# Kernel tuning notes

Hardware: AMD Instinct MI355X
Metric: run time of the kernel (lower is better)

## Reference

```python
import jax, jax.numpy as jnp
import numpy as np

N = 50000          # nodes
E = 800000         # edges (COO)
IN_CH = 128
H1, H2, OUT = 200, 100, 2   # 100*out, 50*out, out with out_channels=2
EPS = 1e-12
DROP_P = 0.1


def setup_inputs() -> dict:
    key = jax.random.key(0)
    ks = jax.random.split(key, 6)
    x = jax.random.normal(ks[0], (N, IN_CH), dtype=jnp.float32)
    edge_index = jax.random.randint(ks[1], (2, E), 0, N)
    W1 = jax.random.normal(ks[2], (IN_CH, H1), dtype=jnp.float32) / np.sqrt(IN_CH)
    W2 = jax.random.normal(ks[3], (H1, H2), dtype=jnp.float32) / np.sqrt(H1)
    W3 = jax.random.normal(ks[4], (H2, OUT), dtype=jnp.float32) / np.sqrt(H2)
    beta1 = jnp.float32(1.0)
    beta2 = jnp.float32(1.0)
    beta3 = jnp.float32(1.0)
    return dict(x=x, edge_index=edge_index, W1=W1, W2=W2, W3=W3,
                beta1=beta1, beta2=beta2, beta3=beta3)


def _agnn_layer(x, W, beta, src, dst):
    # project in -> out channels, then AGNN cosine-attention propagation
    h = x @ W                                               # [N, D]
    hn = h / jnp.maximum(jnp.linalg.norm(h, axis=-1, keepdims=True), EPS)
    a = beta * jnp.sum(hn[src] * hn[dst], axis=-1)          # [E'] edge logits
    amax = jax.ops.segment_max(a, dst, num_segments=N)      # stable segment softmax
    amax = jnp.where(jnp.isfinite(amax), amax, 0.0)
    e = jnp.exp(a - amax[dst])
    denom = jax.ops.segment_sum(e, dst, num_segments=N)
    alpha = e / jnp.maximum(denom[dst], EPS)
    return jax.ops.segment_sum(h[src] * alpha[:, None], dst, num_segments=N)


def _dropout(k, x, p=DROP_P):
    keep = jax.random.bernoulli(k, 1.0 - p, x.shape)
    return jnp.where(keep, x / (1.0 - p), 0.0)


def reference(x, edge_index, W1, W2, W3, beta1, beta2, beta3):
    src, dst = edge_index[0], edge_index[1]
    loop = jnp.arange(N)                                    # self-loops (AGNNConv default)
    src = jnp.concatenate([src, loop])
    dst = jnp.concatenate([dst, loop])
    k1, k2 = jax.random.split(jax.random.key(42))
    h = jax.nn.relu(_agnn_layer(x, W1, beta1, src, dst))
    h = _dropout(k1, h)
    h = jax.nn.relu(_agnn_layer(h, W2, beta2, src, dst))
    h = _dropout(k2, h)
    h = jax.nn.relu(_agnn_layer(h, W3, beta3, src, dst))
    return h
```

## Files before the change

### kernel.cpp

```cpp
#include <hip/hip_runtime.h>
#include <hip/hip_bf16.h>

#define NN 50000
#define NE 800000
#define EPSN 1e-12f


#define H_OFF    0ull
#define A_OFF    40000000ull
#define H3_OFF   80000000ull
#define RINV_OFF 80400000ull
#define OFFS_OFF 80600000ull
#define DEG_OFF  80800016ull
#define CURS_OFF 81000016ull
#define ESRC_OFF 81200016ull
#define CHNK_OFF 84600016ull

__host__ __device__ inline void tf20(unsigned k0, unsigned k1, unsigned& x0, unsigned& x1) {
  unsigned ks2 = k0 ^ k1 ^ 0x1BD11BDAu;
  x0 += k0; x1 += k1;
#define TFR(r) { x0 += x1; x1 = ((x1 << (r)) | (x1 >> (32 - (r)))) ^ x0; }
  TFR(13) TFR(15) TFR(26) TFR(6)
  x0 += k1;  x1 += ks2 + 1u;
  TFR(17) TFR(29) TFR(16) TFR(24)
  x0 += ks2; x1 += k0 + 2u;
  TFR(13) TFR(15) TFR(26) TFR(6)
  x0 += k0;  x1 += k1 + 3u;
  TFR(17) TFR(29) TFR(16) TFR(24)
  x0 += k1;  x1 += ks2 + 4u;
  TFR(13) TFR(15) TFR(26) TFR(6)
  x0 += ks2; x1 += k0 + 5u;
#undef TFR
}

__device__ __forceinline__ float dropf(float val, unsigned k0, unsigned k1, unsigned i) {
  unsigned x0 = 0u, x1 = i;
  tf20(k0, k1, x0, x1);
  unsigned bits = x0 ^ x1;
  float u = __uint_as_float((bits >> 9) | 0x3F800000u) - 1.0f;
  return (u < 0.9f) ? val * (1.0f / 0.9f) : 0.0f;
}

__device__ __forceinline__ float wave_sum(float x) {
  x += __shfl_xor(x, 32); x += __shfl_xor(x, 16); x += __shfl_xor(x, 8);
  x += __shfl_xor(x, 4);  x += __shfl_xor(x, 2);  x += __shfl_xor(x, 1);
  return x;
}

__global__ __launch_bounds__(256) void csr_hist_kernel(const int* __restrict__ ei, int* __restrict__ deg) {
  int e = blockIdx.x * 256 + threadIdx.x;
  if (e >= NE) return;
  atomicAdd(&deg[ei[NE + e]], 1);
}

__global__ __launch_bounds__(256) void csr_scan1_kernel(const int* __restrict__ deg,
                                                        int* __restrict__ offs,
                                                        int* __restrict__ chunk) {
  __shared__ int lds[8];
  int t = threadIdx.x;
  int base = blockIdx.x * 1024 + t * 4;
  int d[4];
#pragma unroll
  for (int j = 0; j < 4; j++) d[j] = (base + j < NN) ? deg[base + j] : 0;
  int ts = d[0] + d[1] + d[2] + d[3];
  int lane = t & 63, wave = t >> 6;
  int inc = ts;
#pragma unroll
  for (int sh = 1; sh < 64; sh <<= 1) { int u = __shfl_up(inc, sh); if (lane >= sh) inc += u; }
  if (lane == 63) lds[wave] = inc;
  __syncthreads();
  if (t == 0) { int s = 0; for (int w = 0; w < 4; w++) { int x = lds[w]; lds[w] = s; s += x; } lds[4] = s; }
  __syncthreads();
  int p = lds[wave] + inc - ts;
#pragma unroll
  for (int j = 0; j < 4; j++) { if (base + j < NN) offs[base + j] = p; p += d[j]; }
  if (t == 255) chunk[blockIdx.x] = lds[4];
}

__global__ __launch_bounds__(64) void csr_scan2_kernel(int* __restrict__ chunk) {
  int t = threadIdx.x;
  int v = (t < 49) ? chunk[t] : 0;
  int inc = v;
#pragma unroll
  for (int sh = 1; sh < 64; sh <<= 1) { int u = __shfl_up(inc, sh); if (t >= sh) inc += u; }
  if (t < 49) chunk[t] = inc - v;
}

__global__ __launch_bounds__(256) void csr_scan3_kernel(int* __restrict__ offs,
                                                        const int* __restrict__ chunk,
                                                        int* __restrict__ curs) {
  int i = blockIdx.x * 256 + threadIdx.x;
  if (i < NN) {
    int val = offs[i] + chunk[i >> 10];
    offs[i] = val;
    curs[i] = val;
  }
  if (i == 0) offs[NN] = NE;
}

__global__ __launch_bounds__(256) void csr_scatter_kernel(const int* __restrict__ ei,
                                                          int* __restrict__ curs,
                                                          int* __restrict__ esrc) {
  int e = blockIdx.x * 256 + threadIdx.x;
  if (e >= NE) return;
  int s = ei[e], d = ei[NE + e];
  int pos = atomicAdd(&curs[d], 1);
  esrc[pos] = s;
}

template<int K, int KT, int NLP, int N>
__device__ __forceinline__ void gemm_body(const float* __restrict__ A,
                                          const float* __restrict__ W,
                                          float* __restrict__ H,
                                          float* __restrict__ RINV, int M) {
  static_assert(NLP % 32 == 0, "NLP must be 32-granular");
  constexpr int KTP = KT + 1, NV = N / 4, NC = NLP / 32, CPT = NC * 4;
  __shared__ float As[64 * KTP];
  __shared__ float Ws[KT * NLP];
  const float4* A4 = (const float4*)A;
  const float4* W4 = (const float4*)W;
  const float4* Ws4 = (const float4*)Ws;

  int t = threadIdx.x, rgrp = t >> 3, cg = t & 7;
  int row0 = blockIdx.x * 64;
  float acc0[CPT], acc1[CPT];
#pragma unroll
  for (int j = 0; j < CPT; j++) { acc0[j] = 0.f; acc1[j] = 0.f; }

  for (int k0 = 0; k0 < K; k0 += KT) {
    __syncthreads();
    for (int idx = t; idx < 64 * (KT / 4); idx += 256) {
      int r = idx / (KT / 4), cq = idx - r * (KT / 4);
      int gr = row0 + r;
      float4 v = (gr < M) ? A4[(size_t)gr * (K / 4) + (k0 / 4) + cq]
                          : make_float4(0.f, 0.f, 0.f, 0.f);
      float* dst = &As[r * KTP + cq * 4];
      dst[0] = v.x; dst[1] = v.y; dst[2] = v.z; dst[3] = v.w;
    }
    for (int idx = t; idx < KT * NV; idx += 256) {
      int kk = idx / NV, cq = idx - kk * NV;
      *(float4*)&Ws[kk * NLP + cq * 4] = W4[(size_t)(k0 + kk) * NV + cq];
    }
    if (NLP > N) {
      for (int idx = t; idx < KT * ((NLP - N) / 4); idx += 256) {
        int kk = idx / ((NLP - N) / 4), cq = idx - kk * ((NLP - N) / 4);
        *(float4*)&Ws[kk * NLP + N + cq * 4] = make_float4(0.f, 0.f, 0.f, 0.f);
      }
    }
    __syncthreads();
#pragma unroll
    for (int kk = 0; kk < KT; kk++) {
      float a0 = As[(rgrp * 2) * KTP + kk];
      float a1 = As[(rgrp * 2 + 1) * KTP + kk];
#pragma unroll
      for (int q = 0; q < NC; q++) {
        float4 wv = Ws4[kk * (NLP / 4) + cg + 8 * q];
        acc0[q * 4 + 0] = fmaf(a0, wv.x, acc0[q * 4 + 0]);
        acc0[q * 4 + 1] = fmaf(a0, wv.y, acc0[q * 4 + 1]);
        acc0[q * 4 + 2] = fmaf(a0, wv.z, acc0[q * 4 + 2]);
        acc0[q * 4 + 3] = fmaf(a0, wv.w, acc0[q * 4 + 3]);
        acc1[q * 4 + 0] = fmaf(a1, wv.x, acc1[q * 4 + 0]);
        acc1[q * 4 + 1] = fmaf(a1, wv.y, acc1[q * 4 + 1]);
        acc1[q * 4 + 2] = fmaf(a1, wv.z, acc1[q * 4 + 2]);
        acc1[q * 4 + 3] = fmaf(a1, wv.w, acc1[q * 4 + 3]);
      }
    }
  }

  int r0 = row0 + rgrp * 2;
#pragma unroll
  for (int rr = 0; rr < 2; rr++) {
    int gr = r0 + rr;
    const float* acc = rr ? acc1 : acc0;
    float ss = 0.f;
#pragma unroll
    for (int q = 0; q < NC; q++) {
#pragma unroll
      for (int j = 0; j < 4; j++) {
        float v = acc[q * 4 + j];
        ss += v * v;
        int c = 4 * (cg + 8 * q) + j;
        if (gr < M && c < N) H[(size_t)gr * N + c] = v;
      }
    }
    ss += __shfl_xor(ss, 1); ss += __shfl_xor(ss, 2); ss += __shfl_xor(ss, 4);
    if (cg == 0 && gr < M) RINV[gr] = 1.0f / fmaxf(sqrtf(ss), EPSN);
  }
}

__global__ __launch_bounds__(256) void gemm1_kernel(const float* A, const float* W,
                                                    float* H, float* RINV, int M) {
  gemm_body<128, 32, 224, 200>(A, W, H, RINV, M);
}
__global__ __launch_bounds__(256) void gemm2_kernel(const float* A, const float* W,
                                                    float* H, float* RINV, int M) {
  gemm_body<200, 40, 128, 100>(A, W, H, RINV, M);
}

template<int D, int VEC, bool DROP>
__device__ __forceinline__ void attn_body(const float* __restrict__ H,
                                          const float* __restrict__ RINV,
                                          const int* __restrict__ OFFS,
                                          const int* __restrict__ ESRC,
                                          const float* __restrict__ BETA,
                                          float* __restrict__ OUT,
                                          unsigned k0, unsigned k1) {
  constexpr int NL = D / VEC;
  int v = blockIdx.x * 4 + (threadIdx.x >> 6);
  int lane = threadIdx.x & 63;
  bool act = lane < NL;
  const float* hrow = H + (size_t)v * D + lane * VEC;
  float hd[VEC];
#pragma unroll
  for (int j = 0; j < VEC; j++) hd[j] = 0.f;
  if (act) {
    if (VEC == 4) { float4 tv = *(const float4*)hrow; hd[0] = tv.x; hd[1] = tv.y; hd[2] = tv.z; hd[3] = tv.w; }
    else          { float2 tv = *(const float2*)hrow; hd[0] = tv.x; hd[1] = tv.y; }
  }
  float beta = BETA[0];
  float bd = beta * RINV[v];
  int e0 = OFFS[v], e1 = OFFS[v + 1];

  float wself = __expf(beta);
  float s = wself;
  float acc[VEC];
#pragma unroll
  for (int j = 0; j < VEC; j++) acc[j] = wself * hd[j];

  int idx = e0;
  for (; idx + 4 <= e1; idx += 4) {
    int   u[4];
    float r[4], dt[4], hs[4][VEC];
#pragma unroll
    for (int m = 0; m < 4; m++) u[m] = ESRC[idx + m];
#pragma unroll
    for (int m = 0; m < 4; m++) r[m] = RINV[u[m]];
#pragma unroll
    for (int m = 0; m < 4; m++) {
      const float* p = H + (size_t)u[m] * D + lane * VEC;
#pragma unroll
      for (int j = 0; j < VEC; j++) hs[m][j] = 0.f;
      if (act) {
        if (VEC == 4) { float4 a = *(const float4*)p; hs[m][0] = a.x; hs[m][1] = a.y; hs[m][2] = a.z; hs[m][3] = a.w; }
        else          { float2 a = *(const float2*)p; hs[m][0] = a.x; hs[m][1] = a.y; }
      }
    }
#pragma unroll
    for (int m = 0; m < 4; m++) {
      float d = 0.f;
#pragma unroll
      for (int j = 0; j < VEC; j++) d = fmaf(hd[j], hs[m][j], d);
      dt[m] = wave_sum(d);
    }
#pragma unroll
    for (int m = 0; m < 4; m++) {
      float w = __expf(bd * dt[m] * r[m]);
      s += w;
#pragma unroll
      for (int j = 0; j < VEC; j++) acc[j] = fmaf(w, hs[m][j], acc[j]);
    }
  }
  for (; idx < e1; ++idx) {
    int u0 = ESRC[idx];
    float r0 = RINV[u0];
    const float* p0 = H + (size_t)u0 * D + lane * VEC;
    float h0[VEC];
#pragma unroll
    for (int j = 0; j < VEC; j++) h0[j] = 0.f;
    if (act) {
      if (VEC == 4) { float4 a = *(const float4*)p0; h0[0] = a.x; h0[1] = a.y; h0[2] = a.z; h0[3] = a.w; }
      else          { float2 a = *(const float2*)p0; h0[0] = a.x; h0[1] = a.y; }
    }
    float d0 = 0.f;
#pragma unroll
    for (int j = 0; j < VEC; j++) d0 = fmaf(hd[j], h0[j], d0);
    d0 = wave_sum(d0);
    float w0 = __expf(bd * d0 * r0);
    s += w0;
#pragma unroll
    for (int j = 0; j < VEC; j++) acc[j] = fmaf(w0, h0[j], acc[j]);
  }

  float rs = 1.0f / fmaxf(s, EPSN);
  if (act) {
    float o[VEC];
#pragma unroll
    for (int j = 0; j < VEC; j++) {
      float val = acc[j] * rs;
      val = (val <= 0.0f) ? 0.0f : val;
      if (DROP) val = dropf(val, k0, k1, (unsigned)(v * D + lane * VEC + j));
      o[j] = val;
    }
    float* orow = OUT + (size_t)v * D + lane * VEC;
    if (VEC == 4) *(float4*)orow = make_float4(o[0], o[1], o[2], o[3]);
    else          *(float2*)orow = make_float2(o[0], o[1]);
  }
}

__global__ __launch_bounds__(256) void attn1_kernel(const float* H, const float* RINV,
                                                    const int* OFFS, const int* ESRC,
                                                    const float* BETA, float* OUT,
                                                    unsigned k0, unsigned k1) {
  attn_body<200, 4, true>(H, RINV, OFFS, ESRC, BETA, OUT, k0, k1);
}
__global__ __launch_bounds__(256) void attn2_kernel(const float* H, const float* RINV,
                                                    const int* OFFS, const int* ESRC,
                                                    const float* BETA, float* OUT,
                                                    unsigned k0, unsigned k1) {
  attn_body<100, 2, true>(H, RINV, OFFS, ESRC, BETA, OUT, k0, k1);
}

__global__ __launch_bounds__(256) void gemm3_kernel(const float* __restrict__ A2,
                                                    const float* __restrict__ W3,
                                                    float* __restrict__ H3,
                                                    float* __restrict__ RINV) {
  __shared__ float w3s[200];
  for (int i = threadIdx.x; i < 200; i += 256) w3s[i] = W3[i];
  __syncthreads();
  int v = blockIdx.x * 256 + threadIdx.x;
  if (v >= NN) return;
  const float* row = A2 + (size_t)v * 100;
  float o0 = 0.f, o1 = 0.f;
#pragma unroll 4
  for (int k = 0; k < 100; k++) {
    float x = row[k];
    o0 = fmaf(x, w3s[2 * k], o0);
    o1 = fmaf(x, w3s[2 * k + 1], o1);
  }
  H3[2 * v] = o0; H3[2 * v + 1] = o1;
  RINV[v] = 1.0f / fmaxf(sqrtf(o0 * o0 + o1 * o1), EPSN);
}

__global__ __launch_bounds__(256) void attn3_kernel(const float* __restrict__ H3,
                                                    const float* __restrict__ RINV,
                                                    const int* __restrict__ OFFS,
                                                    const int* __restrict__ ESRC,
                                                    const float* __restrict__ BETA,
                                                    float* __restrict__ out) {
  int v = blockIdx.x * 4 + (threadIdx.x >> 6);
  int lane = threadIdx.x & 63;
  float beta = BETA[0];
  float bd = beta * RINV[v];
  float h0 = H3[2 * v], h1 = H3[2 * v + 1];
  int e0 = OFFS[v], e1 = OFFS[v + 1];
  float s = 0.f, a0 = 0.f, a1 = 0.f;
  for (int idx = e0 + lane; idx < e1; idx += 64) {
    int u = ESRC[idx];
    float s0 = H3[2 * u], s1 = H3[2 * u + 1];
    float w = __expf(bd * (h0 * s0 + h1 * s1) * RINV[u]);
    s += w; a0 = fmaf(w, s0, a0); a1 = fmaf(w, s1, a1);
  }
  s = wave_sum(s); a0 = wave_sum(a0); a1 = wave_sum(a1);
  if (lane == 0) {
    float wself = __expf(beta);
    s += wself; a0 = fmaf(wself, h0, a0); a1 = fmaf(wself, h1, a1);
    float rs = 1.0f / fmaxf(s, EPSN);
    float o0 = a0 * rs, o1 = a1 * rs;
    out[2 * v]     = (o0 <= 0.0f) ? 0.0f : o0;
    out[2 * v + 1] = (o1 <= 0.0f) ? 0.0f : o1;
  }
}

extern "C" void kernel_launch(void* const* d_in, const int* in_sizes, int n_in,
                              void* d_out, int out_size, void* d_ws, size_t ws_size,
                              hipStream_t stream) {
  const float* X  = (const float*)d_in[0];
  const int*   EI = (const int*)d_in[1];
  const float* W1 = (const float*)d_in[2];
  const float* W2 = (const float*)d_in[3];
  const float* W3 = (const float*)d_in[4];
  const float* B1 = (const float*)d_in[5];
  const float* B2 = (const float*)d_in[6];
  const float* B3 = (const float*)d_in[7];

  char* ws = (char*)d_ws;
  float* H    = (float*)(ws + H_OFF);
  float* A    = (float*)(ws + A_OFF);
  float* H3   = (float*)(ws + H3_OFF);
  float* RINV = (float*)(ws + RINV_OFF);
  int* OFFS   = (int*)(ws + OFFS_OFF);
  int* DEG    = (int*)(ws + DEG_OFF);
  int* CURS   = (int*)(ws + CURS_OFF);
  int* ESRC   = (int*)(ws + ESRC_OFF);
  int* CHNK   = (int*)(ws + CHNK_OFF);

  unsigned k1a = 0u, k1b = 0u; tf20(0u, 42u, k1a, k1b);
  unsigned k2a = 0u, k2b = 1u; tf20(0u, 42u, k2a, k2b);

  hipMemsetAsync(DEG, 0, NN * sizeof(int), stream);
  csr_hist_kernel<<<(NE + 255) / 256, 256, 0, stream>>>(EI, DEG);
  csr_scan1_kernel<<<49, 256, 0, stream>>>(DEG, OFFS, CHNK);
  csr_scan2_kernel<<<1, 64, 0, stream>>>(CHNK);
  csr_scan3_kernel<<<196, 256, 0, stream>>>(OFFS, CHNK, CURS);
  csr_scatter_kernel<<<(NE + 255) / 256, 256, 0, stream>>>(EI, CURS, ESRC);

  const int gb = (NN + 63) / 64;
  const int ab = NN / 4;

  gemm1_kernel<<<gb, 256, 0, stream>>>(X, W1, H, RINV, NN);
  attn1_kernel<<<ab, 256, 0, stream>>>(H, RINV, OFFS, ESRC, B1, A, k1a, k1b);
  gemm2_kernel<<<gb, 256, 0, stream>>>(A, W2, H, RINV, NN);
  attn2_kernel<<<ab, 256, 0, stream>>>(H, RINV, OFFS, ESRC, B2, A, k2a, k2b);
  gemm3_kernel<<<(NN + 255) / 256, 256, 0, stream>>>(A, W3, H3, RINV);
  attn3_kernel<<<ab, 256, 0, stream>>>(H3, RINV, OFFS, ESRC, B3, (float*)d_out);
}
```

Baseline: 503.1 us.

## Fuse degree histogram into first GEMM launch and skip inactive-lane attention work

Merges the CSR degree-histogram pass with the first projection GEMM into one launch, where block IDs past the GEMM tiles run a grid-stride atomic histogram over edges. The two independent jobs can then run concurrently and one launch is saved. The attention kernel is also restructured so inactive lanes skip gather loads and FMAs, and the per-group dot products are computed before the wave reductions to expose more ILP. Shared memory is now one manually partitioned buffer sized for the GEMM, which the histogram blocks also reserve, and uninitialized hd/acc on inactive lanes must never be used.

New measurement: 491.6 us. 2.3% less time.

```diff
diff --git a/kernel.cpp b/kernel.cpp
--- a/kernel.cpp
+++ b/kernel.cpp
@@ -47,82 +47,19 @@
   return x;
 }
 
-__global__ __launch_bounds__(256) void csr_hist_kernel(const int* __restrict__ ei, int* __restrict__ deg) {
-  int e = blockIdx.x * 256 + threadIdx.x;
-  if (e >= NE) return;
-  atomicAdd(&deg[ei[NE + e]], 1);
-}
-
-__global__ __launch_bounds__(256) void csr_scan1_kernel(const int* __restrict__ deg,
-                                                        int* __restrict__ offs,
-                                                        int* __restrict__ chunk) {
-  __shared__ int lds[8];
-  int t = threadIdx.x;
-  int base = blockIdx.x * 1024 + t * 4;
-  int d[4];
-#pragma unroll
-  for (int j = 0; j < 4; j++) d[j] = (base + j < NN) ? deg[base + j] : 0;
-  int ts = d[0] + d[1] + d[2] + d[3];
-  int lane = t & 63, wave = t >> 6;
-  int inc = ts;
-#pragma unroll
-  for (int sh = 1; sh < 64; sh <<= 1) { int u = __shfl_up(inc, sh); if (lane >= sh) inc += u; }
-  if (lane == 63) lds[wave] = inc;
-  __syncthreads();
-  if (t == 0) { int s = 0; for (int w = 0; w < 4; w++) { int x = lds[w]; lds[w] = s; s += x; } lds[4] = s; }
-  __syncthreads();
-  int p = lds[wave] + inc - ts;
-#pragma unroll
-  for (int j = 0; j < 4; j++) { if (base + j < NN) offs[base + j] = p; p += d[j]; }
-  if (t == 255) chunk[blockIdx.x] = lds[4];
-}
-
-__global__ __launch_bounds__(64) void csr_scan2_kernel(int* __restrict__ chunk) {
-  int t = threadIdx.x;
-  int v = (t < 49) ? chunk[t] : 0;
-  int inc = v;
-#pragma unroll
-  for (int sh = 1; sh < 64; sh <<= 1) { int u = __shfl_up(inc, sh); if (t >= sh) inc += u; }
-  if (t < 49) chunk[t] = inc - v;
-}
-
-__global__ __launch_bounds__(256) void csr_scan3_kernel(int* __restrict__ offs,
-                                                        const int* __restrict__ chunk,
-                                                        int* __restrict__ curs) {
-  int i = blockIdx.x * 256 + threadIdx.x;
-  if (i < NN) {
-    int val = offs[i] + chunk[i >> 10];
-    offs[i] = val;
-    curs[i] = val;
-  }
-  if (i == 0) offs[NN] = NE;
-}
-
-__global__ __launch_bounds__(256) void csr_scatter_kernel(const int* __restrict__ ei,
-                                                          int* __restrict__ curs,
-                                                          int* __restrict__ esrc) {
-  int e = blockIdx.x * 256 + threadIdx.x;
-  if (e >= NE) return;
-  int s = ei[e], d = ei[NE + e];
-  int pos = atomicAdd(&curs[d], 1);
-  esrc[pos] = s;
-}
-
 template<int K, int KT, int NLP, int N>
-__device__ __forceinline__ void gemm_body(const float* __restrict__ A,
+__device__ __forceinline__ void gemm_core(float* __restrict__ As, float* __restrict__ Ws,
+                                          const float* __restrict__ A,
                                           const float* __restrict__ W,
                                           float* __restrict__ H,
-                                          float* __restrict__ RINV, int M) {
+                                          float* __restrict__ RINV, int M, int row0) {
   static_assert(NLP % 32 == 0, "NLP must be 32-granular");
   constexpr int KTP = KT + 1, NV = N / 4, NC = NLP / 32, CPT = NC * 4;
-  __shared__ float As[64 * KTP];
-  __shared__ float Ws[KT * NLP];
   const float4* A4 = (const float4*)A;
   const float4* W4 = (const float4*)W;
   const float4* Ws4 = (const float4*)Ws;
 
   int t = threadIdx.x, rgrp = t >> 3, cg = t & 7;
-  int row0 = blockIdx.x * 64;
   float acc0[CPT], acc1[CPT];
 #pragma unroll
   for (int j = 0; j < CPT; j++) { acc0[j] = 0.f; acc1[j] = 0.f; }
@@ -188,13 +125,80 @@
   }
 }
 
-__global__ __launch_bounds__(256) void gemm1_kernel(const float* A, const float* W,
-                                                    float* H, float* RINV, int M) {
-  gemm_body<128, 32, 224, 200>(A, W, H, RINV, M);
-}
+__global__ __launch_bounds__(256) void gemm1_hist_kernel(
+    const float* __restrict__ X, const float* __restrict__ W1,
+    float* __restrict__ H, float* __restrict__ RINV,
+    const int* __restrict__ EI, int* __restrict__ DEG) {
+  __shared__ float smem[9280];
+  int bid = blockIdx.x;
+  if (bid < 782) {
+    gemm_core<128, 32, 224, 200>(smem, smem + 2112, X, W1, H, RINV, NN, bid * 64);
+  } else {
+    for (int e = (bid - 782) * 256 + threadIdx.x; e < NE; e += 242 * 256)
+      atomicAdd(&DEG[EI[NE + e]], 1);
+  }
+}
+
+__global__ __launch_bounds__(256) void csr_scan1_kernel(const int* __restrict__ deg,
+                                                        int* __restrict__ offs,
+                                                        int* __restrict__ chunk) {
+  __shared__ int lds[8];
+  int t = threadIdx.x;
+  int base = blockIdx.x * 1024 + t * 4;
+  int d[4];
+#pragma unroll
+  for (int j = 0; j < 4; j++) d[j] = (base + j < NN) ? deg[base + j] : 0;
+  int ts = d[0] + d[1] + d[2] + d[3];
+  int lane = t & 63, wave = t >> 6;
+  int inc = ts;
+#pragma unroll
+  for (int sh = 1; sh < 64; sh <<= 1) { int u = __shfl_up(inc, sh); if (lane >= sh) inc += u; }
+  if (lane == 63) lds[wave] = inc;
+  __syncthreads();
+  if (t == 0) { int s = 0; for (int w = 0; w < 4; w++) { int x = lds[w]; lds[w] = s; s += x; } lds[4] = s; }
+  __syncthreads();
+  int p = lds[wave] + inc - ts;
+#pragma unroll
+  for (int j = 0; j < 4; j++) { if (base + j < NN) offs[base + j] = p; p += d[j]; }
+  if (t == 255) chunk[blockIdx.x] = lds[4];
+}
+
+__global__ __launch_bounds__(64) void csr_scan2_kernel(int* __restrict__ chunk) {
+  int t = threadIdx.x;
+  int v = (t < 49) ? chunk[t] : 0;
+  int inc = v;
+#pragma unroll
+  for (int sh = 1; sh < 64; sh <<= 1) { int u = __shfl_up(inc, sh); if (t >= sh) inc += u; }
+  if (t < 49) chunk[t] = inc - v;
+}
+
+__global__ __launch_bounds__(256) void csr_scan3_kernel(int* __restrict__ offs,
+                                                        const int* __restrict__ chunk,
+                                                        int* __restrict__ curs) {
+  int i = blockIdx.x * 256 + threadIdx.x;
+  if (i < NN) {
+    int val = offs[i] + chunk[i >> 10];
+    offs[i] = val;
+    curs[i] = val;
+  }
+  if (i == 0) offs[NN] = NE;
+}
+
+__global__ __launch_bounds__(256) void csr_scatter_kernel(const int* __restrict__ ei,
+                                                          int* __restrict__ curs,
+                                                          int* __restrict__ esrc) {
+  int e = blockIdx.x * 256 + threadIdx.x;
+  if (e >= NE) return;
+  int s = ei[e], d = ei[NE + e];
+  int pos = atomicAdd(&curs[d], 1);
+  esrc[pos] = s;
+}
+
 __global__ __launch_bounds__(256) void gemm2_kernel(const float* A, const float* W,
                                                     float* H, float* RINV, int M) {
-  gemm_body<200, 40, 128, 100>(A, W, H, RINV, M);
+  __shared__ float As[64 * 41];
+  __shared__ float Ws[40 * 128];
+  gemm_core<200, 40, 128, 100>(As, Ws, A, W, H, RINV, M, blockIdx.x * 64);
 }
 
 template<int D, int VEC, bool DROP>
@@ -209,23 +213,20 @@
   int v = blockIdx.x * 4 + (threadIdx.x >> 6);
   int lane = threadIdx.x & 63;
   bool act = lane < NL;
-  const float* hrow = H + (size_t)v * D + lane * VEC;
-  float hd[VEC];
-#pragma unroll
-  for (int j = 0; j < VEC; j++) hd[j] = 0.f;
-  if (act) {
-    if (VEC == 4) { float4 tv = *(const float4*)hrow; hd[0] = tv.x; hd[1] = tv.y; hd[2] = tv.z; hd[3] = tv.w; }
-    else          { float2 tv = *(const float2*)hrow; hd[0] = tv.x; hd[1] = tv.y; }
-  }
   float beta = BETA[0];
   float bd = beta * RINV[v];
   int e0 = OFFS[v], e1 = OFFS[v + 1];
 
   float wself = __expf(beta);
   float s = wself;
-  float acc[VEC];
-#pragma unroll
-  for (int j = 0; j < VEC; j++) acc[j] = wself * hd[j];
+  float hd[VEC], acc[VEC];
+  if (act) {
+    const float* hrow = H + (size_t)v * D + lane * VEC;
+    if (VEC == 4) { float4 tv = *(const float4*)hrow; hd[0] = tv.x; hd[1] = tv.y; hd[2] = tv.z; hd[3] = tv.w; }
+    else          { float2 tv = *(const float2*)hrow; hd[0] = tv.x; hd[1] = tv.y; }
+#pragma unroll
+    for (int j = 0; j < VEC; j++) acc[j] = wself * hd[j];
+  }
 
   int idx = e0;
   for (; idx + 4 <= e1; idx += 4) {
@@ -235,50 +236,50 @@
     for (int m = 0; m < 4; m++) u[m] = ESRC[idx + m];
 #pragma unroll
     for (int m = 0; m < 4; m++) r[m] = RINV[u[m]];
-#pragma unroll
-    for (int m = 0; m < 4; m++) {
-      const float* p = H + (size_t)u[m] * D + lane * VEC;
-#pragma unroll
-      for (int j = 0; j < VEC; j++) hs[m][j] = 0.f;
-      if (act) {
+    float dd[4] = {0.f, 0.f, 0.f, 0.f};
+    if (act) {
+#pragma unroll
+      for (int m = 0; m < 4; m++) {
+        const float* p = H + (size_t)u[m] * D + lane * VEC;
         if (VEC == 4) { float4 a = *(const float4*)p; hs[m][0] = a.x; hs[m][1] = a.y; hs[m][2] = a.z; hs[m][3] = a.w; }
         else          { float2 a = *(const float2*)p; hs[m][0] = a.x; hs[m][1] = a.y; }
       }
-    }
-#pragma unroll
-    for (int m = 0; m < 4; m++) {
-      float d = 0.f;
-#pragma unroll
-      for (int j = 0; j < VEC; j++) d = fmaf(hd[j], hs[m][j], d);
-      dt[m] = wave_sum(d);
-    }
-#pragma unroll
-    for (int m = 0; m < 4; m++) {
-      float w = __expf(bd * dt[m] * r[m]);
-      s += w;
-#pragma unroll
-      for (int j = 0; j < VEC; j++) acc[j] = fmaf(w, hs[m][j], acc[j]);
+#pragma unroll
+      for (int m = 0; m < 4; m++)
+#pragma unroll
+        for (int j = 0; j < VEC; j++) dd[m] = fmaf(hd[j], hs[m][j], dd[m]);
+    }
+#pragma unroll
+    for (int m = 0; m < 4; m++) dt[m] = wave_sum(dd[m]);
+    float w[4];
+#pragma unroll
+    for (int m = 0; m < 4; m++) { w[m] = __expf(bd * dt[m] * r[m]); s += w[m]; }
+    if (act) {
+#pragma unroll
+      for (int m = 0; m < 4; m++)
+#pragma unroll
+        for (int j = 0; j < VEC; j++) acc[j] = fmaf(w[m], hs[m][j], acc[j]);
     }
   }
   for (; idx < e1; ++idx) {
     int u0 = ESRC[idx];
     float r0 = RINV[u0];
-    const float* p0 = H + (size_t)u0 * D + lane * VEC;
     float h0[VEC];
-#pragma unroll
-    for (int j = 0; j < VEC; j++) h0[j] = 0.f;
+    float ddt = 0.f;
     if (act) {
+      const float* p0 = H + (size_t)u0 * D + lane * VEC;
       if (VEC == 4) { float4 a = *(const float4*)p0; h0[0] = a.x; h0[1] = a.y; h0[2] = a.z; h0[3] = a.w; }
       else          { float2 a = *(const float2*)p0; h0[0] = a.x; h0[1] = a.y; }
-    }
-    float d0 = 0.f;
-#pragma unroll
-    for (int j = 0; j < VEC; j++) d0 = fmaf(hd[j], h0[j], d0);
-    d0 = wave_sum(d0);
-    float w0 = __expf(bd * d0 * r0);
+#pragma unroll
+      for (int j = 0; j < VEC; j++) ddt = fmaf(hd[j], h0[j], ddt);
+    }
+    ddt = wave_sum(ddt);
+    float w0 = __expf(bd * ddt * r0);
     s += w0;
-#pragma unroll
-    for (int j = 0; j < VEC; j++) acc[j] = fmaf(w0, h0[j], acc[j]);
+    if (act) {
+#pragma unroll
+      for (int j = 0; j < VEC; j++) acc[j] = fmaf(w0, h0[j], acc[j]);
+    }
   }
 
   float rs = 1.0f / fmaxf(s, EPSN);
@@ -388,7 +389,8 @@
   unsigned k2a = 0u, k2b = 1u; tf20(0u, 42u, k2a, k2b);
 
   hipMemsetAsync(DEG, 0, NN * sizeof(int), stream);
-  csr_hist_kernel<<<(NE + 255) / 256, 256, 0, stream>>>(EI, DEG);
+
+  gemm1_hist_kernel<<<1024, 256, 0, stream>>>(X, W1, H, RINV, EI, DEG);
   csr_scan1_kernel<<<49, 256, 0, stream>>>(DEG, OFFS, CHNK);
   csr_scan2_kernel<<<1, 64, 0, stream>>>(CHNK);
   csr_scan3_kernel<<<196, 256, 0, stream>>>(OFFS, CHNK, CURS);
@@ -397,7 +399,6 @@
   const int gb = (NN + 63) / 64;
   const int ab = NN / 4;
 
-  gemm1_kernel<<<gb, 256, 0, stream>>>(X, W1, H, RINV, NN);
   attn1_kernel<<<ab, 256, 0, stream>>>(H, RINV, OFFS, ESRC, B1, A, k1a, k1b);
   gemm2_kernel<<<gb, 256, 0, stream>>>(A, W2, H, RINV, NN);
   attn2_kernel<<<ab, 256, 0, stream>>>(H, RINV, OFFS, ESRC, B2, A, k2a, k2b);
```
